# Performance work log

Measured on AMD Instinct MI355X. Metric: run time of the kernel, lower is better.

Reference implementation:

```python
import jax, jax.numpy as jnp
import numpy as np

PATCH = 16
MIN_MASK_RATIO = 0.5
DIST_THRESHOLD = 0.5
BSEARCH_STEPS = 10


def _patchify(img, p):
    # (N, C, H, W) -> (N, L, p*p*C), matching torch permute(0,2,4,3,5,1)
    N, C, H, W = img.shape
    x = img.reshape(N, C, H // p, p, W // p, p)
    x = x.transpose(0, 2, 4, 3, 5, 1)
    return x.reshape(N, (H // p) * (W // p), p * p * C)


def setup_inputs() -> dict:
    key = jax.random.key(0)
    img = jax.random.normal(key, (32, 3, 512, 512), dtype=jnp.float32)
    return {"img": img, "mask_ratio_pct": 75}


def reference(img, mask_ratio_pct):
    mask_ratio = mask_ratio_pct / 100.0  # static python float (0.75)
    patches = _patchify(img, PATCH)  # (N, L, D)
    N, L, D = patches.shape

    # normalize_patches: per-patch mean/std (torch std is unbiased, ddof=1)
    mean = patches.mean(axis=-1, keepdims=True)
    std = patches.std(axis=-1, ddof=1, keepdims=True) + 1e-6
    normp = (patches - mean) / std

    # F.normalize(p=2, dim=-1) then bmm -> cosine similarity (N, L, L)
    pn = normp / jnp.maximum(
        jnp.linalg.norm(normp, axis=-1, keepdims=True), 1e-12)
    sim = jnp.einsum('nld,nmd->nlm', pn, pn)

    # select_anchors: static count, random indices
    num_anchors = max(1, int(L * mask_ratio * 0.05))
    k_anchor, k_add = jax.random.split(jax.random.key(42))
    anchor_idx = jax.random.permutation(k_anchor, L)[:num_anchors]

    # adjust_threshold: 10-step binary search on global mask ratio
    target = jnp.float32(mask_ratio)

    def body(i, st):
        left, right, best_t, best_d = st
        thr = (left + right) * 0.5
        ratio = jnp.mean(jnp.any(sim > thr, axis=-1).astype(jnp.float32))
        diff = jnp.abs(ratio - target)
        better = diff < best_d
        best_t = jnp.where(better, thr, best_t)
        best_d = jnp.where(better, diff, best_d)
        gt = ratio > target
        left = jnp.where(gt, thr, left)
        right = jnp.where(gt, right, thr)
        return (left, right, best_t, best_d)

    st0 = (jnp.float32(0.0), jnp.float32(1.0),
           jnp.float32(DIST_THRESHOLD), jnp.float32(jnp.inf))
    _, _, thr, _ = jax.lax.fori_loop(0, BSEARCH_STEPS, body, st0)

    # mask: any anchor similarity above threshold (N, L)
    anchor_sim = sim[:, anchor_idx, :]  # (N, A, L)
    mask = jnp.any(anchor_sim > thr, axis=1)

    # per-sample min-ratio correction: add random unmasked patches
    ratio = mask.astype(jnp.float32).mean(axis=1)  # (N,)
    n_add = jnp.where(ratio < MIN_MASK_RATIO,
                      jnp.floor((MIN_MASK_RATIO - ratio) * L),
                      0.0).astype(jnp.int32)  # (N,)
    # random priority among unmasked positions; masked -> +inf (never first)
    keys_u = jax.random.uniform(k_add, (N, L), dtype=jnp.float32)
    keys_u = jnp.where(mask, jnp.inf, keys_u)
    order = jnp.argsort(keys_u, axis=1)
    rank = jnp.argsort(order, axis=1)  # rank of each position in random order
    additional = rank < n_add[:, None]
    return mask | additional
```

## Files before the change

### kernel.cpp

```cpp
#include <hip/hip_runtime.h>

typedef unsigned int u32;
typedef __attribute__((ext_vector_type(8))) short bf16x8;
typedef __attribute__((ext_vector_type(4))) float f32x4;

#define TF_PART 1

#define META_OFF 0
#define SK_OFF   4096
#define MASK_OFF 16384
#define SUMA_OFF (MASK_OFF + 131072)
#define FRAG_OFF (SUMA_OFF + 32*64*4)

__device__ __forceinline__ void tf2x32(u32 k0, u32 k1, u32 x0, u32 x1, u32& o0, u32& o1) {
  const u32 ks2 = k0 ^ k1 ^ 0x1BD11BDAu;
  u32 v0 = x0 + k0, v1 = x1 + k1;
#define TFR(r) { v0 += v1; v1 = (v1 << (r)) | (v1 >> (32 - (r))); v1 ^= v0; }
  TFR(13) TFR(15) TFR(26) TFR(6)   v0 += k1;  v1 += ks2 + 1u;
  TFR(17) TFR(29) TFR(16) TFR(24)  v0 += ks2; v1 += k0 + 2u;
  TFR(13) TFR(15) TFR(26) TFR(6)   v0 += k0;  v1 += k1 + 3u;
  TFR(17) TFR(29) TFR(16) TFR(24)  v0 += k1;  v1 += ks2 + 4u;
  TFR(13) TFR(15) TFR(26) TFR(6)   v0 += ks2; v1 += k0 + 5u;
#undef TFR
  o0 = v0; o1 = v1;
}

__device__ __forceinline__ float bits_to_unit(u32 b) {
  return __uint_as_float((b >> 9) | 0x3f800000u) - 1.0f;
}

__device__ __forceinline__ ushort f2bf(float f) {
  u32 b = __float_as_uint(f);
  return (ushort)((b + 0x7fffu + ((b >> 16) & 1u)) >> 16);
}

__global__ void k0a_setup(const int* __restrict__ pct, int* __restrict__ meta,
                          u32* __restrict__ sk_g) {
  __shared__ u32 sub0, sub1;
  const int t = threadIdx.x;
  if (t == 0) {
    u32 ka0, ka1, kb0, kb1, s0, s1;
#if TF_PART
    tf2x32(0u, 42u, 0u, 0u, ka0, ka1);
    tf2x32(0u, 42u, 0u, 1u, kb0, kb1);
    tf2x32(ka0, ka1, 0u, 1u, s0, s1);
#else
    u32 a, b, c, d;
    tf2x32(0u, 42u, 0u, 2u, a, b);
    tf2x32(0u, 42u, 1u, 3u, c, d);
    ka0 = a; ka1 = c; kb0 = b; kb1 = d;
    tf2x32(ka0, ka1, 0u, 2u, a, b);
    tf2x32(ka0, ka1, 1u, 3u, c, d);
    s0 = b; s1 = d;
#endif
    meta[1] = (int)kb0; meta[2] = (int)kb1;
    sub0 = s0; sub1 = s1;
    const int p = pct[0];
    int na = (int)(1024.0 * ((double)p / 100.0) * 0.05);
    if (na < 1) na = 1;
    if (na > 64) na = 64;
    meta[0] = na;
  }
  __syncthreads();
#if TF_PART
  { u32 o0, o1; tf2x32(sub0, sub1, 0u, (u32)t, o0, o1); sk_g[t] = o0 ^ o1; }
#else
  if (t < 512) {
    u32 o0, o1; tf2x32(sub0, sub1, (u32)t, (u32)(t + 512), o0, o1);
    sk_g[t] = o0; sk_g[t + 512] = o1;
  }
#endif
}

__global__ void k0b_rank(const int* __restrict__ meta, const u32* __restrict__ sk_g,
                         int* __restrict__ meta_anchor) {
  __shared__ __align__(16) u32 sk_[1024];
  const int t = threadIdx.x;
#pragma unroll
  for (int i = 0; i < 16; ++i) sk_[t + 64 * i] = sk_g[t + 64 * i];
  __syncthreads();
  const int idx = blockIdx.x * 64 + t;
  const u32 mine = sk_[idx];
  const int na = meta[0];
  int rank = 0;
  const uint4* s4 = (const uint4*)sk_;
#pragma unroll 4
  for (int j = 0; j < 256; ++j) {
    const uint4 v = s4[j];
    const int m = j * 4;
    rank += (v.x < mine || (v.x == mine && m < idx));
    rank += (v.y < mine || (v.y == mine && m + 1 < idx));
    rank += (v.z < mine || (v.z == mine && m + 2 < idx));
    rank += (v.w < mine || (v.w == mine && m + 3 < idx));
  }
  if (rank < na) meta_anchor[rank] = idx;
}

__device__ __forceinline__ void load_patch(const float* __restrict__ img, int n, int ph, int pw,
                                           int lane, float4 v[3]) {
  const int py = lane >> 2;
  const int px = (lane & 3) << 2;
  const float* b = img + (size_t)n * 786432 + (size_t)(ph * 16 + py) * 512 + pw * 16 + px;
#pragma unroll
  for (int c = 0; c < 3; ++c)
    v[c] = *reinterpret_cast<const float4*>(b + (size_t)c * 262144);
}

__device__ __forceinline__ float wred(float v) {
#pragma unroll
  for (int k = 32; k >= 1; k >>= 1) v += __shfl_xor(v, k);
  return v;
}

__device__ __forceinline__ float red4(float a0, float a1, float a2, float a3, int lane) {
  a0 += __shfl_xor(a0, 32); a0 += __shfl_xor(a0, 16);
  a1 += __shfl_xor(a1, 32); a1 += __shfl_xor(a1, 16);
  a2 += __shfl_xor(a2, 32); a2 += __shfl_xor(a2, 16);
  a3 += __shfl_xor(a3, 32); a3 += __shfl_xor(a3, 16);
  const int g = lane >> 4;
  float v = g == 0 ? a0 : (g == 1 ? a1 : (g == 2 ? a2 : a3));
  v += __shfl_xor(v, 8);
  v += __shfl_xor(v, 4);
  v += __shfl_xor(v, 2);
  v += __shfl_xor(v, 1);
  return v;
}

__device__ __forceinline__ float sum4(float4 a) { return a.x + a.y + a.z + a.w; }

__global__ void k2_anchor(const float* __restrict__ img, const int* __restrict__ meta,
                          float* __restrict__ sumA, ushort* __restrict__ fragA) {
  __shared__ __align__(16) float pns[4][768];
  const int lane = threadIdx.x & 63;
  const int wid = threadIdx.x >> 6;
  const int wg = blockIdx.x * 4 + wid;
  const int n = wg >> 6, a = wg & 63;
  const int na = meta[0];
  const int mt = a >> 4, row = a & 15;
  const bool valid = a < na;
  if (valid) {
    const int m = meta[4 + a];
    const int ph = m >> 5, pw = m & 31;
    float4 v[3];
    load_patch(img, n, ph, pw, lane, v);
    float s = sum4(v[0]) + sum4(v[1]) + sum4(v[2]);
    s = wred(s);
    const float mu = s * (1.0f / 768.0f);
    float q = 0.0f;
#pragma unroll
    for (int c = 0; c < 3; ++c) {
      float dx = v[c].x - mu; q += dx * dx;
      dx = v[c].y - mu; q += dx * dx;
      dx = v[c].z - mu; q += dx * dx;
      dx = v[c].w - mu; q += dx * dx;
    }
    q = wred(q);
    const float inv = 1.0f / sqrtf(q);
    float sa = 0.0f;
    float4 o[3];
#pragma unroll
    for (int c = 0; c < 3; ++c) {
      o[c].x = (v[c].x - mu) * inv; sa += o[c].x;
      o[c].y = (v[c].y - mu) * inv; sa += o[c].y;
      o[c].z = (v[c].z - mu) * inv; sa += o[c].z;
      o[c].w = (v[c].w - mu) * inv; sa += o[c].w;
    }
    sa = wred(sa);
    float4* dst = reinterpret_cast<float4*>(pns[wid]);
    dst[lane] = o[0]; dst[lane + 64] = o[1]; dst[lane + 128] = o[2];
    if (lane == 0) sumA[n * 64 + a] = sa;
  } else {
    if (lane == 0) sumA[n * 64 + a] = 0.0f;
  }
  __syncthreads();
#pragma unroll
  for (int it = 0; it < 2; ++it) {
    const int s = lane + it * 64;
    if (s < 96) {
      const int kk = s >> 2, g = s & 3;
      uint4 w = {0u, 0u, 0u, 0u};
      if (valid) {
        const float* src = pns[wid] + kk * 32 + g * 8;
        const float4 v0 = *(const float4*)src;
        const float4 v1 = *(const float4*)(src + 4);
        w.x = (u32)f2bf(v0.x) | ((u32)f2bf(v0.y) << 16);
        w.y = (u32)f2bf(v0.z) | ((u32)f2bf(v0.w) << 16);
        w.z = (u32)f2bf(v1.x) | ((u32)f2bf(v1.y) << 16);
        w.w = (u32)f2bf(v1.z) | ((u32)f2bf(v1.w) << 16);
      }
      *(uint4*)(fragA + ((size_t)(((n * 4 + mt) * 24 + kk) * 64) + g * 16 + row) * 8) = w;
    }
  }
}

__global__ __launch_bounds__(256) void k3_mfma(const float* __restrict__ img,
                                               const ushort* __restrict__ fragA,
                                               const float* __restrict__ sumA,
                                               int* __restrict__ mask) {
  __shared__ float smu[64], srs[64];
  const int lane = threadIdx.x & 63;
  const int w = threadIdx.x >> 6;
  const int n = blockIdx.x >> 4, tile = blockIdx.x & 15;
  const int pbase = tile * 64 + w * 16;
#pragma unroll
  for (int sg = 0; sg < 4; ++sg) {
    const int p0 = pbase + sg * 4;
    const int ph = p0 >> 5, pw0 = p0 & 31;
    float4 pv[4][3];
#pragma unroll
    for (int p = 0; p < 4; ++p) load_patch(img, n, ph, pw0 + p, lane, pv[p]);
    float s0 = sum4(pv[0][0]) + sum4(pv[0][1]) + sum4(pv[0][2]);
    float s1 = sum4(pv[1][0]) + sum4(pv[1][1]) + sum4(pv[1][2]);
    float s2 = sum4(pv[2][0]) + sum4(pv[2][1]) + sum4(pv[2][2]);
    float s3 = sum4(pv[3][0]) + sum4(pv[3][1]) + sum4(pv[3][2]);
    float sv = red4(s0, s1, s2, s3, lane);
    const float mu0 = __shfl(sv, 0) * (1.0f / 768.0f);
    const float mu1 = __shfl(sv, 16) * (1.0f / 768.0f);
    const float mu2 = __shfl(sv, 32) * (1.0f / 768.0f);
    const float mu3 = __shfl(sv, 48) * (1.0f / 768.0f);
    float q0 = 0, q1 = 0, q2 = 0, q3 = 0;
#pragma unroll
    for (int c = 0; c < 3; ++c) {
      float d;
      d = pv[0][c].x - mu0; q0 += d * d; d = pv[0][c].y - mu0; q0 += d * d;
      d = pv[0][c].z - mu0; q0 += d * d; d = pv[0][c].w - mu0; q0 += d * d;
      d = pv[1][c].x - mu1; q1 += d * d; d = pv[1][c].y - mu1; q1 += d * d;
      d = pv[1][c].z - mu1; q1 += d * d; d = pv[1][c].w - mu1; q1 += d * d;
      d = pv[2][c].x - mu2; q2 += d * d; d = pv[2][c].y - mu2; q2 += d * d;
      d = pv[2][c].z - mu2; q2 += d * d; d = pv[2][c].w - mu2; q2 += d * d;
      d = pv[3][c].x - mu3; q3 += d * d; d = pv[3][c].y - mu3; q3 += d * d;
      d = pv[3][c].z - mu3; q3 += d * d; d = pv[3][c].w - mu3; q3 += d * d;
    }
    const float qv = red4(q0, q1, q2, q3, lane);
    const int g = lane >> 4;
    if ((lane & 15) == 0) {
      const float mug = g == 0 ? mu0 : (g == 1 ? mu1 : (g == 2 ? mu2 : mu3));
      smu[w * 16 + sg * 4 + g] = mug;
      srs[w * 16 + sg * 4 + g] = 1.0f / sqrtf(qv);
    }
  }
  __syncthreads();
  const int c = lane & 15, g = lane >> 4;
  const int p = pbase + c;
  const int ph = p >> 5, pw = p & 31;
  const float* imgn = img + (size_t)n * 786432;
  f32x4 acc[4];
#pragma unroll
  for (int mt = 0; mt < 4; ++mt) acc[mt] = (f32x4){0.f, 0.f, 0.f, 0.f};
  const ushort* fbase = fragA + (size_t)(n * 4) * 24 * 512;
  for (int kk = 0; kk < 24; ++kk) {
    const int e0 = kk * 32 + g * 8;
    const int cch = e0 >> 8, rem = e0 & 255, py = rem >> 4, px = rem & 15;
    const float* bsrc = imgn + (size_t)cch * 262144 + (size_t)(ph * 16 + py) * 512 + pw * 16 + px;
    const float4 b0 = *(const float4*)bsrc;
    const float4 b1 = *(const float4*)(bsrc + 4);
    bf16x8 bf;
    bf[0] = (short)f2bf(b0.x); bf[1] = (short)f2bf(b0.y);
    bf[2] = (short)f2bf(b0.z); bf[3] = (short)f2bf(b0.w);
    bf[4] = (short)f2bf(b1.x); bf[5] = (short)f2bf(b1.y);
    bf[6] = (short)f2bf(b1.z); bf[7] = (short)f2bf(b1.w);
#pragma unroll
    for (int mt = 0; mt < 4; ++mt) {
      const bf16x8 af = *(const bf16x8*)(fbase + ((size_t)(mt * 24 + kk) * 64 + lane) * 8);
      acc[mt] = __builtin_amdgcn_mfma_f32_16x16x32_bf16(af, bf, acc[mt], 0, 0, 0);
    }
  }
  const float mu_c = smu[w * 16 + c];
  const float rs_c = srs[w * 16 + c];
  int fl = 0;
#pragma unroll
  for (int mt = 0; mt < 4; ++mt) {
    const float4 s4 = *(const float4*)(sumA + n * 64 + mt * 16 + g * 4);
    float sim;
    sim = (acc[mt][0] - mu_c * s4.x) * rs_c; fl |= (sim > 0.5f) ? 1 : 0;
    sim = (acc[mt][1] - mu_c * s4.y) * rs_c; fl |= (sim > 0.5f) ? 1 : 0;
    sim = (acc[mt][2] - mu_c * s4.z) * rs_c; fl |= (sim > 0.5f) ? 1 : 0;
    sim = (acc[mt][3] - mu_c * s4.w) * rs_c; fl |= (sim > 0.5f) ? 1 : 0;
  }
  fl |= __shfl_xor(fl, 16);
  fl |= __shfl_xor(fl, 32);
  if (lane < 16) mask[n * 1024 + p] = fl;
}

__global__ void k4_final(const int* __restrict__ meta, const int* __restrict__ mask,
                         int* __restrict__ out) {
  __shared__ __align__(16) float ks_[1024];
  __shared__ int cnt_s;
  const int nimg = blockIdx.x >> 2, seg = blockIdx.x & 3, t = threadIdx.x;
  if (t == 0) cnt_s = 0;
  __syncthreads();
  const u32 k0 = (u32)meta[1], k1 = (u32)meta[2];
  const int base = nimg * 1024;
  const float INF = __int_as_float(0x7f800000);
  int local = 0;
#pragma unroll
  for (int i = 0; i < 4; ++i) {
    const int j = t + 256 * i;
    const int gi = base + j;
    const int mk = mask[gi];
    u32 o0, o1; float u;
#if TF_PART
    tf2x32(k0, k1, 0u, (u32)gi, o0, o1);
    u = bits_to_unit(o0 ^ o1);
#else
    if (gi < 16384) { tf2x32(k0, k1, (u32)gi, (u32)(gi + 16384), o0, o1); u = bits_to_unit(o0); }
    else            { tf2x32(k0, k1, (u32)(gi - 16384), (u32)gi, o0, o1); u = bits_to_unit(o1); }
#endif
    ks_[j] = mk ? INF : u;
    local += mk;
  }
#pragma unroll
  for (int k = 32; k >= 1; k >>= 1) local += __shfl_xor(local, k);
  if ((t & 63) == 0) atomicAdd(&cnt_s, local);
  __syncthreads();
  const int cnt = cnt_s;
  const int nadd = cnt < 512 ? (512 - cnt) : 0;
  const int l = seg * 256 + t;
  const float kl = ks_[l];
  const int mk_l = mask[base + l];
  int rank = 0;
  const float4* s4 = (const float4*)ks_;
#pragma unroll 4
  for (int j = 0; j < 256; ++j) {
    const float4 v = s4[j];
    const int m = j * 4;
    rank += (v.x < kl || (v.x == kl && m < l));
    rank += (v.y < kl || (v.y == kl && m + 1 < l));
    rank += (v.z < kl || (v.z == kl && m + 2 < l));
    rank += (v.w < kl || (v.w == kl && m + 3 < l));
  }
  out[base + l] = (mk_l || rank < nadd) ? 1 : 0;
}

extern "C" void kernel_launch(void* const* d_in, const int* in_sizes, int n_in,
                              void* d_out, int out_size, void* d_ws, size_t ws_size,
                              hipStream_t stream) {
  const float* img = (const float*)d_in[0];
  const int* pct = (const int*)d_in[1];
  char* ws = (char*)d_ws;
  int* meta = (int*)(ws + META_OFF);
  u32* sk_g = (u32*)(ws + SK_OFF);
  int* mask = (int*)(ws + MASK_OFF);
  float* sumA = (float*)(ws + SUMA_OFF);
  ushort* fragA = (ushort*)(ws + FRAG_OFF);
  int* out = (int*)d_out;

  hipLaunchKernelGGL(k0a_setup, dim3(1), dim3(1024), 0, stream, pct, meta, sk_g);
  hipLaunchKernelGGL(k0b_rank, dim3(16), dim3(64), 0, stream, meta, sk_g, meta + 4);
  hipLaunchKernelGGL(k2_anchor, dim3(512), dim3(256), 0, stream, img, meta, sumA, fragA);
  hipLaunchKernelGGL(k3_mfma, dim3(512), dim3(256), 0, stream, img, fragA, sumA, mask);
  hipLaunchKernelGGL(k4_final, dim3(128), dim3(256), 0, stream, meta, mask, out);
}
```

Measured before the change: 222.2 us.

## Fuse patch mean/variance stats into MFMA loop, removing separate stats pass

```diff
diff --git a/kernel.cpp b/kernel.cpp
--- a/kernel.cpp
+++ b/kernel.cpp
@@ -112,20 +112,6 @@
   return v;
 }
 
-__device__ __forceinline__ float red4(float a0, float a1, float a2, float a3, int lane) {
-  a0 += __shfl_xor(a0, 32); a0 += __shfl_xor(a0, 16);
-  a1 += __shfl_xor(a1, 32); a1 += __shfl_xor(a1, 16);
-  a2 += __shfl_xor(a2, 32); a2 += __shfl_xor(a2, 16);
-  a3 += __shfl_xor(a3, 32); a3 += __shfl_xor(a3, 16);
-  const int g = lane >> 4;
-  float v = g == 0 ? a0 : (g == 1 ? a1 : (g == 2 ? a2 : a3));
-  v += __shfl_xor(v, 8);
-  v += __shfl_xor(v, 4);
-  v += __shfl_xor(v, 2);
-  v += __shfl_xor(v, 1);
-  return v;
-}
-
 __device__ __forceinline__ float sum4(float4 a) { return a.x + a.y + a.z + a.w; }
 
 __global__ void k2_anchor(const float* __restrict__ img, const int* __restrict__ meta,
@@ -197,85 +183,60 @@
                                                const ushort* __restrict__ fragA,
                                                const float* __restrict__ sumA,
                                                int* __restrict__ mask) {
-  __shared__ float smu[64], srs[64];
   const int lane = threadIdx.x & 63;
   const int w = threadIdx.x >> 6;
   const int n = blockIdx.x >> 4, tile = blockIdx.x & 15;
   const int pbase = tile * 64 + w * 16;
-#pragma unroll
-  for (int sg = 0; sg < 4; ++sg) {
-    const int p0 = pbase + sg * 4;
-    const int ph = p0 >> 5, pw0 = p0 & 31;
-    float4 pv[4][3];
-#pragma unroll
-    for (int p = 0; p < 4; ++p) load_patch(img, n, ph, pw0 + p, lane, pv[p]);
-    float s0 = sum4(pv[0][0]) + sum4(pv[0][1]) + sum4(pv[0][2]);
-    float s1 = sum4(pv[1][0]) + sum4(pv[1][1]) + sum4(pv[1][2]);
-    float s2 = sum4(pv[2][0]) + sum4(pv[2][1]) + sum4(pv[2][2]);
-    float s3 = sum4(pv[3][0]) + sum4(pv[3][1]) + sum4(pv[3][2]);
-    float sv = red4(s0, s1, s2, s3, lane);
-    const float mu0 = __shfl(sv, 0) * (1.0f / 768.0f);
-    const float mu1 = __shfl(sv, 16) * (1.0f / 768.0f);
-    const float mu2 = __shfl(sv, 32) * (1.0f / 768.0f);
-    const float mu3 = __shfl(sv, 48) * (1.0f / 768.0f);
-    float q0 = 0, q1 = 0, q2 = 0, q3 = 0;
-#pragma unroll
-    for (int c = 0; c < 3; ++c) {
-      float d;
-      d = pv[0][c].x - mu0; q0 += d * d; d = pv[0][c].y - mu0; q0 += d * d;
-      d = pv[0][c].z - mu0; q0 += d * d; d = pv[0][c].w - mu0; q0 += d * d;
-      d = pv[1][c].x - mu1; q1 += d * d; d = pv[1][c].y - mu1; q1 += d * d;
-      d = pv[1][c].z - mu1; q1 += d * d; d = pv[1][c].w - mu1; q1 += d * d;
-      d = pv[2][c].x - mu2; q2 += d * d; d = pv[2][c].y - mu2; q2 += d * d;
-      d = pv[2][c].z - mu2; q2 += d * d; d = pv[2][c].w - mu2; q2 += d * d;
-      d = pv[3][c].x - mu3; q3 += d * d; d = pv[3][c].y - mu3; q3 += d * d;
-      d = pv[3][c].z - mu3; q3 += d * d; d = pv[3][c].w - mu3; q3 += d * d;
-    }
-    const float qv = red4(q0, q1, q2, q3, lane);
-    const int g = lane >> 4;
-    if ((lane & 15) == 0) {
-      const float mug = g == 0 ? mu0 : (g == 1 ? mu1 : (g == 2 ? mu2 : mu3));
-      smu[w * 16 + sg * 4 + g] = mug;
-      srs[w * 16 + sg * 4 + g] = 1.0f / sqrtf(qv);
-    }
-  }
-  __syncthreads();
   const int c = lane & 15, g = lane >> 4;
   const int p = pbase + c;
   const int ph = p >> 5, pw = p & 31;
   const float* imgn = img + (size_t)n * 786432;
-  f32x4 acc[4];
-#pragma unroll
-  for (int mt = 0; mt < 4; ++mt) acc[mt] = (f32x4){0.f, 0.f, 0.f, 0.f};
+  f32x4 a0 = {0.f, 0.f, 0.f, 0.f}, a1 = {0.f, 0.f, 0.f, 0.f};
+  f32x4 a2 = {0.f, 0.f, 0.f, 0.f}, a3 = {0.f, 0.f, 0.f, 0.f};
+  float s = 0.0f, q = 0.0f;
   const ushort* fbase = fragA + (size_t)(n * 4) * 24 * 512;
+#pragma unroll 4
   for (int kk = 0; kk < 24; ++kk) {
     const int e0 = kk * 32 + g * 8;
     const int cch = e0 >> 8, rem = e0 & 255, py = rem >> 4, px = rem & 15;
     const float* bsrc = imgn + (size_t)cch * 262144 + (size_t)(ph * 16 + py) * 512 + pw * 16 + px;
     const float4 b0 = *(const float4*)bsrc;
     const float4 b1 = *(const float4*)(bsrc + 4);
+    s += b0.x + b0.y + b0.z + b0.w + b1.x + b1.y + b1.z + b1.w;
+    q = fmaf(b0.x, b0.x, q); q = fmaf(b0.y, b0.y, q);
+    q = fmaf(b0.z, b0.z, q); q = fmaf(b0.w, b0.w, q);
+    q = fmaf(b1.x, b1.x, q); q = fmaf(b1.y, b1.y, q);
+    q = fmaf(b1.z, b1.z, q); q = fmaf(b1.w, b1.w, q);
     bf16x8 bf;
     bf[0] = (short)f2bf(b0.x); bf[1] = (short)f2bf(b0.y);
     bf[2] = (short)f2bf(b0.z); bf[3] = (short)f2bf(b0.w);
     bf[4] = (short)f2bf(b1.x); bf[5] = (short)f2bf(b1.y);
     bf[6] = (short)f2bf(b1.z); bf[7] = (short)f2bf(b1.w);
-#pragma unroll
-    for (int mt = 0; mt < 4; ++mt) {
-      const bf16x8 af = *(const bf16x8*)(fbase + ((size_t)(mt * 24 + kk) * 64 + lane) * 8);
-      acc[mt] = __builtin_amdgcn_mfma_f32_16x16x32_bf16(af, bf, acc[mt], 0, 0, 0);
-    }
-  }
-  const float mu_c = smu[w * 16 + c];
-  const float rs_c = srs[w * 16 + c];
+    const ushort* fk = fbase + (size_t)kk * 512 + (size_t)lane * 8;
+    const bf16x8 af0 = *(const bf16x8*)(fk);
+    const bf16x8 af1 = *(const bf16x8*)(fk + 24 * 512);
+    const bf16x8 af2 = *(const bf16x8*)(fk + 48 * 512);
+    const bf16x8 af3 = *(const bf16x8*)(fk + 72 * 512);
+    a0 = __builtin_amdgcn_mfma_f32_16x16x32_bf16(af0, bf, a0, 0, 0, 0);
+    a1 = __builtin_amdgcn_mfma_f32_16x16x32_bf16(af1, bf, a1, 0, 0, 0);
+    a2 = __builtin_amdgcn_mfma_f32_16x16x32_bf16(af2, bf, a2, 0, 0, 0);
+    a3 = __builtin_amdgcn_mfma_f32_16x16x32_bf16(af3, bf, a3, 0, 0, 0);
+  }
+  s += __shfl_xor(s, 16); s += __shfl_xor(s, 32);
+  q += __shfl_xor(q, 16); q += __shfl_xor(q, 32);
+  const float mu_c = s * (1.0f / 768.0f);
+  const float qc = q - s * s * (1.0f / 768.0f);
+  const float rs_c = 1.0f / sqrtf(qc);
   int fl = 0;
 #pragma unroll
   for (int mt = 0; mt < 4; ++mt) {
+    const f32x4 acc = mt == 0 ? a0 : (mt == 1 ? a1 : (mt == 2 ? a2 : a3));
     const float4 s4 = *(const float4*)(sumA + n * 64 + mt * 16 + g * 4);
     float sim;
-    sim = (acc[mt][0] - mu_c * s4.x) * rs_c; fl |= (sim > 0.5f) ? 1 : 0;
-    sim = (acc[mt][1] - mu_c * s4.y) * rs_c; fl |= (sim > 0.5f) ? 1 : 0;
-    sim = (acc[mt][2] - mu_c * s4.z) * rs_c; fl |= (sim > 0.5f) ? 1 : 0;
-    sim = (acc[mt][3] - mu_c * s4.w) * rs_c; fl |= (sim > 0.5f) ? 1 : 0;
+    sim = (acc[0] - mu_c * s4.x) * rs_c; fl |= (sim > 0.5f) ? 1 : 0;
+    sim = (acc[1] - mu_c * s4.y) * rs_c; fl |= (sim > 0.5f) ? 1 : 0;
+    sim = (acc[2] - mu_c * s4.z) * rs_c; fl |= (sim > 0.5f) ? 1 : 0;
+    sim = (acc[3] - mu_c * s4.w) * rs_c; fl |= (sim > 0.5f) ? 1 : 0;
   }
   fl |= __shfl_xor(fl, 16);
   fl |= __shfl_xor(fl, 32);
```

After: 207.3 us. -6.7%, faster.
